# Kernel optimization log

Measured on AMD Instinct MI355X. Metric: run time of the kernel, lower is better.

The kernel has to match this reference:

```python
import jax, jax.numpy as jnp
import numpy as np

N, E, H, G, NF, L = 50000, 600000, 128, 50, 128, 6
NC, NM = 500, 100  # conformers, molecules
CUTOFF = 10.0
OFFSET = jnp.linspace(0.0, CUTOFF, G)                 # GaussianSmearing offsets
COEFF = -0.5 / (CUTOFF / (G - 1)) ** 2
LOG2 = float(np.log(2.0))

def ssp(x):  # ShiftedSoftplus
    return jax.nn.softplus(x) - LOG2

def setup_inputs() -> dict:
    key = jax.random.key(0)
    ks = jax.random.split(key, 24)
    s = 0.05
    return {
        'z': jax.random.randint(ks[0], (N,), 0, 120),
        'pos': jax.random.normal(ks[1], (N, 3), jnp.float32) * 5.0,
        'edge_row': jax.random.randint(ks[2], (E,), 0, N),   # source j
        'edge_col': jax.random.randint(ks[3], (E,), 0, N),   # target i
        'atom_to_conf': jnp.sort(jax.random.randint(ks[4], (N,), 0, NC)),
        'conf_to_mol': jnp.sort(jax.random.randint(ks[5], (NC,), 0, NM)),
        'emb_table': jax.random.normal(ks[6], (120, H)) * s,
        'mlp_w1': jax.random.normal(ks[7], (L, G, NF)) * s,
        'mlp_b1': jnp.zeros((L, NF)),
        'mlp_w2': jax.random.normal(ks[8], (L, NF, NF)) * s,
        'mlp_b2': jnp.zeros((L, NF)),
        'conv_lin1_w': jax.random.normal(ks[9], (L, H, NF)) * s,
        'conv_lin2_w': jax.random.normal(ks[10], (L, NF, H)) * s,
        'conv_lin2_b': jnp.zeros((L, H)),
        'int_lin_w': jax.random.normal(ks[11], (L, H, H)) * s,
        'int_lin_b': jnp.zeros((L, H)),
        'lin1_w': jax.random.normal(ks[12], (H, H)) * s,
        'lin1_b': jnp.zeros((H,)),
        'lin2_w': jax.random.normal(ks[13], (H, H)) * s,
        'lin2_b': jnp.zeros((H,)),
        'head_w1': jax.random.normal(ks[14], (H, H // 2)) * s,
        'head_b1': jnp.zeros((H // 2,)),
        'head_w2': jax.random.normal(ks[15], (H // 2, 1)) * s,
        'head_b2': jnp.zeros((1,)),
    }

def reference(z, pos, edge_row, edge_col, atom_to_conf, conf_to_mol,
              emb_table, mlp_w1, mlp_b1, mlp_w2, mlp_b2,
              conv_lin1_w, conv_lin2_w, conv_lin2_b, int_lin_w, int_lin_b,
              lin1_w, lin1_b, lin2_w, lin2_b,
              head_w1, head_b1, head_w2, head_b2):
    h = emb_table[z]                                         # [N,H]
    # edge geometry (radius graph distances)
    d = jnp.linalg.norm(pos[edge_row] - pos[edge_col], axis=-1)       # [E]
    edge_attr = jnp.exp(COEFF * (d[:, None] - OFFSET[None, :]) ** 2)  # [E,G]
    C = 0.5 * (jnp.cos(d * jnp.pi / CUTOFF) + 1.0)                    # [E]
    for i in range(L):
        # filter network + cosine cutoff
        W = ssp(edge_attr @ mlp_w1[i] + mlp_b1[i]) @ mlp_w2[i] + mlp_b2[i]
        W = W * C[:, None]                                   # [E,NF]
        xf = h @ conv_lin1_w[i]                              # [N,NF]
        msg = xf[edge_row] * W                               # gather x_j, multiply
        agg = jax.ops.segment_sum(msg, edge_col, num_segments=N)  # scatter-add
        x = agg @ conv_lin2_w[i] + conv_lin2_b[i]
        x = ssp(x) @ int_lin_w[i] + int_lin_b[i]
        h = h + x                                            # residual
    h = ssp(h @ lin1_w + lin1_b) @ lin2_w + lin2_b           # [N,H]
    conf_emb = jax.ops.segment_sum(h, atom_to_conf, num_segments=NC)  # [NC,H]
    mol_emb = jax.ops.segment_sum(conf_emb, conf_to_mol, num_segments=NM)  # [NM,H]
    out = (ssp(mol_emb @ head_w1 + head_b1) @ head_w2 + head_b2)[:, 0]  # [NM]
    return out
```

## Files before the change

kernel.cpp:

```cpp
#include <hip/hip_runtime.h>
#include <hip/hip_bf16.h>
#include <hip/hip_fp16.h>
#include <math.h>

#define H_DIM   128
#define NF_DIM  128
#define G_DIM   50
#define L_LAYERS 6
#define TBL     2048
#define DMAX    12.8f
#define CUTOFF_C 10.0f
#define COEFF_C (-0.5f * 49.0f * 49.0f / 100.0f)
#define SCAN_B  256
#define T_PER   16
#define T_PER2  (T_PER + 1)
#define STG_STR 140

typedef __bf16 bf16x8 __attribute__((ext_vector_type(8)));
typedef float  f32x4  __attribute__((ext_vector_type(4)));

__device__ __forceinline__ float sspf(float x) {
    float e = __expf(-fabsf(x));
    return fmaxf(x, 0.0f) + __logf(1.0f + e) - 0.69314718055994530942f;
}

__device__ __forceinline__ unsigned short f2bf(float f) {
    unsigned int u = __float_as_uint(f);
    u = (u + 0x7fffu + ((u >> 16) & 1u)) >> 16;
    return (unsigned short)u;
}

__device__ __forceinline__ float bf2f(unsigned short u) {
    return __uint_as_float(((unsigned int)u) << 16);
}

__device__ __forceinline__ int swz(int c) {
    return c ^ ((c >> 3) & 7) ^ ((c >> 8) & 3);
}

__global__ __launch_bounds__(128) void build_tables(
        const float* __restrict__ w1, const float* __restrict__ b1,
        const float* __restrict__ w2, const float* __restrict__ b2,
        unsigned int* __restrict__ tab2) {
    int l  = blockIdx.x / (TBL / T_PER);
    int t0 = (blockIdx.x % (TBL / T_PER)) * T_PER;
    int f  = threadIdx.x;
    __shared__ float sW1[G_DIM * 128];
    __shared__ float gs[T_PER2][G_DIM + 2];
    __shared__ float sy[T_PER2][130];
    for (int i = f; i < G_DIM * 128; i += 128)
        sW1[i] = w1[(size_t)l * G_DIM * 128 + i];
    if (f < G_DIM) {
        float o = f * (CUTOFF_C / (G_DIM - 1));
#pragma unroll
        for (int u = 0; u < T_PER2; ++u) {
            int t = t0 + u;
            if (t > TBL - 1) t = TBL - 1;
            float dt = t * (DMAX / (TBL - 1));
            float dd = dt - o;
            gs[u][f] = __expf(COEFF_C * dd * dd);
        }
    }
    __syncthreads();
    float y[T_PER2];
    float bb = b1[l * 128 + f];
#pragma unroll
    for (int u = 0; u < T_PER2; ++u) y[u] = bb;
    for (int g = 0; g < G_DIM; ++g) {
        float wv = sW1[g * 128 + f];
#pragma unroll
        for (int u = 0; u < T_PER2; ++u) y[u] += gs[u][g] * wv;
    }
#pragma unroll
    for (int u = 0; u < T_PER2; ++u) sy[u][f] = sspf(y[u]);
    __syncthreads();
    float acc[T_PER2];
    float b2v = b2[l * 128 + f];
#pragma unroll
    for (int u = 0; u < T_PER2; ++u) acc[u] = b2v;
    const float* W2 = w2 + (size_t)l * 16384;
    for (int k = 0; k < 128; ++k) {
        float wv = W2[k * 128 + f];
#pragma unroll
        for (int u = 0; u < T_PER2; ++u) acc[u] += sy[u][k] * wv;
    }
#pragma unroll
    for (int u = 0; u < T_PER; ++u) {
        unsigned int lo = f2bf(acc[u]);
        unsigned int hi = f2bf(acc[u + 1]);
        tab2[((size_t)l * TBL + t0 + u) * 128 + f] = (hi << 16) | lo;
    }
}

__global__ __launch_bounds__(256) void embed_kernel(
        const int* __restrict__ z, const float* __restrict__ emb,
        float* __restrict__ h, int N) {
    int idx = blockIdx.x * blockDim.x + threadIdx.x;
    if (idx >= N * H_DIM) return;
    int n = idx >> 7, f = idx & 127;
    h[idx] = emb[z[n] * H_DIM + f];
}

__global__ __launch_bounds__(256) void prep_wt_sw(
        const float* __restrict__ W, unsigned short* __restrict__ Bsw) {
    int m = blockIdx.x;
    const float* src = W + (size_t)m * 16384;
    unsigned short* dst = Bsw + (size_t)m * 16384;
    for (int i = threadIdx.x; i < 16384; i += 256) {
        int jj = i & 7, lane = (i >> 3) & 63, j = (i >> 9) & 7, ks = i >> 12;
        int n = j * 16 + (lane & 15);
        int k = ks * 32 + ((lane >> 4) & 3) * 8 + jj;
        dst[i] = f2bf(src[k * 128 + n]);
    }
}

__global__ __launch_bounds__(256) void count_kernel(
        const int* __restrict__ ec, int* __restrict__ cnt,
        int* __restrict__ rank, int E) {
    int e = blockIdx.x * blockDim.x + threadIdx.x;
    if (e < E) rank[e] = atomicAdd(&cnt[ec[e]], 1);
}

__global__ __launch_bounds__(SCAN_B) void scan1(
        const int* __restrict__ cnt, int* __restrict__ excl,
        int* __restrict__ bsums, int N) {
    __shared__ int s[SCAN_B];
    int i = blockIdx.x * SCAN_B + threadIdx.x;
    int v = (i < N) ? cnt[i] : 0;
    s[threadIdx.x] = v;
    __syncthreads();
    for (int off = 1; off < SCAN_B; off <<= 1) {
        int t = (threadIdx.x >= off) ? s[threadIdx.x - off] : 0;
        __syncthreads();
        s[threadIdx.x] += t;
        __syncthreads();
    }
    if (i < N) excl[i] = s[threadIdx.x] - v;
    if (threadIdx.x == SCAN_B - 1) bsums[blockIdx.x] = s[SCAN_B - 1];
}

__global__ __launch_bounds__(SCAN_B) void scan2(int* __restrict__ bsums, int nb) {
    __shared__ int s[SCAN_B];
    int v = (threadIdx.x < nb) ? bsums[threadIdx.x] : 0;
    s[threadIdx.x] = v;
    __syncthreads();
    for (int off = 1; off < SCAN_B; off <<= 1) {
        int t = (threadIdx.x >= off) ? s[threadIdx.x - off] : 0;
        __syncthreads();
        s[threadIdx.x] += t;
        __syncthreads();
    }
    if (threadIdx.x < nb) bsums[threadIdx.x] = s[threadIdx.x] - v;
}

__global__ __launch_bounds__(SCAN_B) void scan3(
        const int* __restrict__ excl, const int* __restrict__ bsums,
        int* __restrict__ row_start, int N, int E) {
    int i = blockIdx.x * SCAN_B + threadIdx.x;
    if (i < N) row_start[i] = excl[i] + bsums[blockIdx.x];
    if (i == 0) row_start[N] = E;
}

__global__ __launch_bounds__(256) void build_edges(
        const int* __restrict__ er, const int* __restrict__ ec,
        const float* __restrict__ pos, const int* __restrict__ row_start,
        const int* __restrict__ rank, uint2* __restrict__ ebuf, int E) {
    int e = blockIdx.x * blockDim.x + threadIdx.x;
    if (e >= E) return;
    int r = er[e], c = ec[e];
    float dx = pos[r * 3 + 0] - pos[c * 3 + 0];
    float dy = pos[r * 3 + 1] - pos[c * 3 + 1];
    float dz = pos[r * 3 + 2] - pos[c * 3 + 2];
    float d = sqrtf(dx * dx + dy * dy + dz * dz);
    float C = 0.5f * (cosf(d * (3.14159265358979323846f / CUTOFF_C)) + 1.0f);
    float t = fminf(d, DMAX) * ((TBL - 1) / DMAX);
    int i0 = (int)t;
    if (i0 > TBL - 2) i0 = TBL - 2;
    float fr = t - (float)i0;
    __half2 abh = __floats2half2_rn(C * (1.0f - fr), C * fr);
    ebuf[row_start[c] + rank[e]] =
        make_uint2((unsigned)r | ((unsigned)i0 << 17), *(unsigned*)&abh);
}

__device__ __forceinline__ void edge_acc(
        unsigned ex, unsigned ey, const unsigned int* __restrict__ tab2,
        const unsigned short* __restrict__ xfb, int f4, float4& acc) {
    int r = ex & 0x1ffff, i0 = ex >> 17;
    float2 ab = __half22float2(*(__half2*)&ey);
    uint4 tp = *(const uint4*)(tab2 + (size_t)i0 * 128 + f4);
    const ushort4 xu = *(const ushort4*)(xfb + (size_t)r * 128 + f4);
    acc.x += bf2f(xu.x) * (ab.x * __uint_as_float(tp.x << 16) +
                           ab.y * __uint_as_float(tp.x & 0xffff0000u));
    acc.y += bf2f(xu.y) * (ab.x * __uint_as_float(tp.y << 16) +
                           ab.y * __uint_as_float(tp.y & 0xffff0000u));
    acc.z += bf2f(xu.z) * (ab.x * __uint_as_float(tp.z << 16) +
                           ab.y * __uint_as_float(tp.z & 0xffff0000u));
    acc.w += bf2f(xu.w) * (ab.x * __uint_as_float(tp.w << 16) +
                           ab.y * __uint_as_float(tp.w & 0xffff0000u));
}

__global__ __launch_bounds__(256) void edge_agg(
        const uint2* __restrict__ ebuf, const int* __restrict__ row_start,
        const unsigned short* __restrict__ xfb, const unsigned int* __restrict__ tab2,
        unsigned short* __restrict__ aggb, int N) {
    int tid = threadIdx.x;
    int atom = blockIdx.x * 8 + (tid >> 5);
    if (atom >= N) return;
    int f4 = (tid & 31) * 4;
    float4 a0 = make_float4(0.f, 0.f, 0.f, 0.f);
    float4 a1 = make_float4(0.f, 0.f, 0.f, 0.f);
    float4 a2 = make_float4(0.f, 0.f, 0.f, 0.f);
    float4 a3 = make_float4(0.f, 0.f, 0.f, 0.f);
    int j0 = row_start[atom], j1 = row_start[atom + 1];
    int j = j0;
    if (j < j1 && (j & 1)) {
        uint2 ed = ebuf[j];
        edge_acc(ed.x, ed.y, tab2, xfb, f4, a0);
        ++j;
    }
    for (; j + 3 < j1; j += 4) {
        uint4 e2 = *(const uint4*)(ebuf + j);
        uint4 e3 = *(const uint4*)(ebuf + j + 2);
        edge_acc(e2.x, e2.y, tab2, xfb, f4, a0);
        edge_acc(e2.z, e2.w, tab2, xfb, f4, a1);
        edge_acc(e3.x, e3.y, tab2, xfb, f4, a2);
        edge_acc(e3.z, e3.w, tab2, xfb, f4, a3);
    }
    if (j + 1 < j1) {
        uint4 e2 = *(const uint4*)(ebuf + j);
        edge_acc(e2.x, e2.y, tab2, xfb, f4, a0);
        edge_acc(e2.z, e2.w, tab2, xfb, f4, a1);
        j += 2;
    }
    if (j < j1) {
        uint2 ed = ebuf[j];
        edge_acc(ed.x, ed.y, tab2, xfb, f4, a0);
    }
    a0.x += a1.x + a2.x + a3.x;
    a0.y += a1.y + a2.y + a3.y;
    a0.z += a1.z + a2.z + a3.z;
    a0.w += a1.w + a2.w + a3.w;
    unsigned short o[4] = {f2bf(a0.x), f2bf(a0.y), f2bf(a0.z), f2bf(a0.w)};
    *(uint2*)(aggb + (size_t)atom * 128 + f4) = *(const uint2*)o;
}

#define MODE_BIAS     1
#define MODE_SSP_OUT  2
#define MODE_OUT_BF16 4

__global__ __launch_bounds__(256, 4) void gemm_v2(
        const float* __restrict__ A, const unsigned short* __restrict__ Bsw,
        const float* __restrict__ bias, float* __restrict__ OutF,
        unsigned short* __restrict__ OutB, int M, int mode) {
    __shared__ __align__(16) float smem[64 * 132];
    unsigned short* asw = (unsigned short*)smem;
    int tid = threadIdx.x;
    int m0 = blockIdx.x * 64;

    for (int i = tid; i < 1024; i += 256) {
        int ks = i >> 8, w = (i >> 6) & 3, ln = i & 63;
        int row = m0 + w * 16 + (ln & 15);
        int kb = ks * 32 + (ln >> 4) * 8;
        unsigned short tmp[8];
        if (row < M) {
            const float* ap = A + (size_t)row * 128 + kb;
            float4 v0 = *(const float4*)ap;
            float4 v1 = *(const float4*)(ap + 4);
            tmp[0] = f2bf(v0.x); tmp[1] = f2bf(v0.y);
            tmp[2] = f2bf(v0.z); tmp[3] = f2bf(v0.w);
            tmp[4] = f2bf(v1.x); tmp[5] = f2bf(v1.y);
            tmp[6] = f2bf(v1.z); tmp[7] = f2bf(v1.w);
        } else {
#pragma unroll
            for (int j = 0; j < 8; ++j) tmp[j] = 0;
        }
        *(uint4*)(asw + (size_t)i * 8) = *(const uint4*)tmp;
    }
    __syncthreads();

    int w = tid >> 6, ln = tid & 63;
    int quad = ln >> 4, l15 = ln & 15;
    f32x4 acc[8] = {};
#pragma unroll
    for (int ks = 0; ks < 4; ++ks) {
        bf16x8 af = *(const bf16x8*)(asw + ((ks * 4 + w) * 64 + ln) * 8);
#pragma unroll
        for (int j = 0; j < 8; ++j) {
            bf16x8 bf = *(const bf16x8*)(Bsw + (((ks * 8 + j) * 64) + ln) * 8);
            acc[j] = __builtin_amdgcn_mfma_f32_16x16x32_bf16(af, bf, acc[j], 0, 0, 0);
        }
    }
    __syncthreads();

#pragma unroll
    for (int j = 0; j < 8; ++j) {
        int col = j * 16 + l15;
        float bv = (mode & MODE_BIAS) ? bias[col] : 0.f;
#pragma unroll
        for (int r = 0; r < 4; ++r)
            smem[(w * 16 + quad * 4 + r) * 132 + col] = acc[j][r] + bv;
    }
    __syncthreads();

    for (int i = tid; i < 2048; i += 256) {
        int row = i >> 5, c4 = (i & 31) * 4;
        int grow = m0 + row;
        if (grow >= M) continue;
        float4 v = *(const float4*)(smem + row * 132 + c4);
        if (mode & MODE_SSP_OUT) {
            v.x = sspf(v.x); v.y = sspf(v.y); v.z = sspf(v.z); v.w = sspf(v.w);
        }
        if (mode & MODE_OUT_BF16) {
            unsigned short o[4] = {f2bf(v.x), f2bf(v.y), f2bf(v.z), f2bf(v.w)};
            *(uint2*)(OutB + (size_t)grow * 128 + c4) = *(const uint2*)o;
        } else {
            *(float4*)(OutF + (size_t)grow * 128 + c4) = v;
        }
    }
}

__global__ __launch_bounds__(256, 4) void fused_layer(
        const unsigned short* __restrict__ aggb,
        const unsigned short* __restrict__ B1sw, const float* __restrict__ b1v,
        const unsigned short* __restrict__ B2sw, const float* __restrict__ b2v,
        const unsigned short* __restrict__ B3sw, const float* __restrict__ b3v,
        float* __restrict__ h, unsigned short* __restrict__ xfb_next,
        float* __restrict__ s_out, int M, int last) {
    __shared__ __align__(16) unsigned short frag[8192];
    __shared__ __align__(16) unsigned short stg[64 * STG_STR];
    int tid = threadIdx.x;
    int m0 = blockIdx.x * 64;

    for (int i = tid; i < 1024; i += 256) {
        int ks = i >> 8, w_ = (i >> 6) & 3, ln_ = i & 63;
        int row = m0 + w_ * 16 + (ln_ & 15);
        int kb = ks * 32 + (ln_ >> 4) * 8;
        uint4 v = make_uint4(0, 0, 0, 0);
        if (row < M) v = *(const uint4*)(aggb + (size_t)row * 128 + kb);
        *(uint4*)(frag + swz(i) * 8) = v;
    }
    __syncthreads();

    int w = tid >> 6, ln = tid & 63;
    int quad = ln >> 4, l15 = ln & 15;

    f32x4 acc[8] = {};
#pragma unroll
    for (int ks = 0; ks < 4; ++ks) {
        bf16x8 af = *(const bf16x8*)(frag + swz((ks * 4 + w) * 64 + ln) * 8);
#pragma unroll
        for (int j = 0; j < 8; ++j) {
            bf16x8 bf = *(const bf16x8*)(B1sw + (((ks * 8 + j) * 64) + ln) * 8);
            acc[j] = __builtin_amdgcn_mfma_f32_16x16x32_bf16(af, bf, acc[j], 0, 0, 0);
        }
    }

#pragma unroll
    for (int j = 0; j < 8; ++j) {
        int col = j * 16 + l15;
        float bv = b1v[col];
        int ks2 = j >> 1;
        int quad2 = (col >> 3) & 3;
        int jj = l15 & 7;
        int cbase = (ks2 * 4 + w) * 64 + quad2 * 16 + quad * 4;
#pragma unroll
        for (int r = 0; r < 4; ++r) {
            float s = sspf(acc[j][r] + bv);
            frag[swz(cbase + r) * 8 + jj] = f2bf(s);
        }
    }

    f32x4 acc2[8] = {};
#pragma unroll
    for (int ks = 0; ks < 4; ++ks) {
        bf16x8 af = *(const bf16x8*)(frag + swz((ks * 4 + w) * 64 + ln) * 8);
#pragma unroll
        for (int j = 0; j < 8; ++j) {
            bf16x8 bf = *(const bf16x8*)(B2sw + (((ks * 8 + j) * 64) + ln) * 8);
            acc2[j] = __builtin_amdgcn_mfma_f32_16x16x32_bf16(af, bf, acc2[j], 0, 0, 0);
        }
    }

#pragma unroll
    for (int j = 0; j < 8; ++j) {
        int col = j * 16 + l15;
        float bv = b2v[col];
#pragma unroll
        for (int r = 0; r < 4; ++r)
            stg[(w * 16 + quad * 4 + r) * STG_STR + col] = f2bf(acc2[j][r] + bv);
    }
    __syncthreads();

    for (int i = tid; i < 2048; i += 256) {
        int row = i >> 5, c4 = (i & 31) * 4;
        int grow = m0 + row;
        ushort4 xv = *(const ushort4*)(stg + row * STG_STR + c4);
        float4 v;
        v.x = bf2f(xv.x); v.y = bf2f(xv.y); v.z = bf2f(xv.z); v.w = bf2f(xv.w);
        if (grow < M) {
            float* hp = h + (size_t)grow * 128 + c4;
            float4 o = *(const float4*)hp;
            v.x += o.x; v.y += o.y; v.z += o.z; v.w += o.w;
            *(float4*)hp = v;
        } else {
            v = make_float4(0.f, 0.f, 0.f, 0.f);
        }
        unsigned short t4[4] = {f2bf(v.x), f2bf(v.y), f2bf(v.z), f2bf(v.w)};
        int w_ = row >> 4, l15_ = row & 15;
        int ks = c4 >> 5, q_ = (c4 >> 3) & 3, jj = c4 & 7;
        int c = (ks * 4 + w_) * 64 + q_ * 16 + l15_;
        *(uint2*)(frag + swz(c) * 8 + jj) = *(const uint2*)t4;
    }
    __syncthreads();

    f32x4 acc3[8] = {};
#pragma unroll
    for (int ks = 0; ks < 4; ++ks) {
        bf16x8 af = *(const bf16x8*)(frag + swz((ks * 4 + w) * 64 + ln) * 8);
#pragma unroll
        for (int j = 0; j < 8; ++j) {
            bf16x8 bf = *(const bf16x8*)(B3sw + (((ks * 8 + j) * 64) + ln) * 8);
            acc3[j] = __builtin_amdgcn_mfma_f32_16x16x32_bf16(af, bf, acc3[j], 0, 0, 0);
        }
    }

#pragma unroll
    for (int j = 0; j < 8; ++j) {
        int col = j * 16 + l15;
        float bv = last ? b3v[col] : 0.f;
#pragma unroll
        for (int r = 0; r < 4; ++r) {
            float v = acc3[j][r] + bv;
            if (last) v = sspf(v);
            stg[(w * 16 + quad * 4 + r) * STG_STR + col] = f2bf(v);
        }
    }
    __syncthreads();

    for (int i = tid; i < 2048; i += 256) {
        int row = i >> 5, c4 = (i & 31) * 4;
        int grow = m0 + row;
        if (grow >= M) continue;
        ushort4 s4 = *(const ushort4*)(stg + row * STG_STR + c4);
        if (last) {
            float4 v;
            v.x = bf2f(s4.x); v.y = bf2f(s4.y); v.z = bf2f(s4.z); v.w = bf2f(s4.w);
            *(float4*)(s_out + (size_t)grow * 128 + c4) = v;
        } else {
            *(uint2*)(xfb_next + (size_t)grow * 128 + c4) = *(const uint2*)&s4;
        }
    }
}

#define MR_ATOMS 32
__global__ __launch_bounds__(128) void mol_reduce(
        const float* __restrict__ s, const int* __restrict__ a2c,
        const int* __restrict__ c2m, float* __restrict__ mols,
        int* __restrict__ cnt, int N) {
    int f = threadIdx.x;
    int a0 = blockIdx.x * MR_ATOMS;
    int a1 = min(a0 + MR_ATOMS, N);
    float sum = 0.f;
    int cur = -1, run = 0;
    for (int a = a0; a < a1; ++a) {
        int m = c2m[a2c[a]];
        if (m != cur) {
            if (cur >= 0) {
                unsafeAtomicAdd(&mols[(size_t)cur * H_DIM + f], sum);
                if (f == 0) atomicAdd(&cnt[cur], run);
            }
            cur = m; sum = 0.f; run = 0;
        }
        sum += s[(size_t)a * H_DIM + f];
        ++run;
    }
    if (cur >= 0) {
        unsafeAtomicAdd(&mols[(size_t)cur * H_DIM + f], sum);
        if (f == 0) atomicAdd(&cnt[cur], run);
    }
}

__global__ __launch_bounds__(128) void head_kernel(
        const float* __restrict__ mols, const int* __restrict__ cnt,
        const float* __restrict__ l2w, const float* __restrict__ l2b,
        const float* __restrict__ hw1, const float* __restrict__ hb1,
        const float* __restrict__ hw2, const float* __restrict__ hb2,
        float* __restrict__ out) {
    int m = blockIdx.x, f = threadIdx.x;
    __shared__ float me[H_DIM];
    __shared__ float u[H_DIM / 2];
    const float* ms = mols + (size_t)m * H_DIM;
    float acc = l2b[f] * (float)cnt[m];
#pragma unroll 16
    for (int k = 0; k < H_DIM; ++k) acc += ms[k] * l2w[k * H_DIM + f];
    me[f] = acc;
    __syncthreads();
    if (f < 64) {
        float a2 = hb1[f];
#pragma unroll 16
        for (int k = 0; k < H_DIM; ++k) a2 += me[k] * hw1[k * 64 + f];
        u[f] = sspf(a2);
    }
    __syncthreads();
    if (f == 0) {
        float o = hb2[0];
#pragma unroll 16
        for (int j = 0; j < 64; ++j) o += u[j] * hw2[j];
        out[m] = o;
    }
}

extern "C" void kernel_launch(void* const* d_in, const int* in_sizes, int n_in,
                              void* d_out, int out_size, void* d_ws, size_t ws_size,
                              hipStream_t stream) {
    const int*   z   = (const int*)d_in[0];
    const float* pos = (const float*)d_in[1];
    const int*   er  = (const int*)d_in[2];
    const int*   ec  = (const int*)d_in[3];
    const int*   a2c = (const int*)d_in[4];
    const int*   c2m = (const int*)d_in[5];
    const float* emb = (const float*)d_in[6];
    const float* w1  = (const float*)d_in[7];
    const float* b1  = (const float*)d_in[8];
    const float* w2  = (const float*)d_in[9];
    const float* b2  = (const float*)d_in[10];
    const float* c1w = (const float*)d_in[11];
    const float* c2w = (const float*)d_in[12];
    const float* c2b = (const float*)d_in[13];
    const float* iw  = (const float*)d_in[14];
    const float* ib  = (const float*)d_in[15];
    const float* l1w = (const float*)d_in[16];
    const float* l1b = (const float*)d_in[17];
    const float* l2w = (const float*)d_in[18];
    const float* l2b = (const float*)d_in[19];
    const float* hw1 = (const float*)d_in[20];
    const float* hb1 = (const float*)d_in[21];
    const float* hw2 = (const float*)d_in[22];
    const float* hb2 = (const float*)d_in[23];

    const int N  = in_sizes[0];
    const int E  = in_sizes[2];
    const int NM = out_size;
    float* out = (float*)d_out;

    char* wsp = (char*)d_ws;
    uint2* ebuf = (uint2*)wsp;            wsp += (size_t)E * 8;
    unsigned int* tab2 = (unsigned int*)wsp;  wsp += (size_t)L_LAYERS * TBL * NF_DIM * 4;
    unsigned short* wbt = (unsigned short*)wsp;  wsp += (size_t)19 * 16384 * 2;
    float* h    = (float*)wsp;            wsp += (size_t)N * H_DIM * 4;
    unsigned short* xfb = (unsigned short*)wsp;  wsp += (size_t)N * H_DIM * 2;
    unsigned short* aggb = (unsigned short*)wsp; wsp += (size_t)N * H_DIM * 2;
    float* sbuf = (float*)wsp;            wsp += (size_t)N * H_DIM * 4;
    float* mols = (float*)wsp;            wsp += (size_t)NM * H_DIM * 4;
    int*   cnt_m = (int*)wsp;             wsp += (size_t)NM * 4;
    int*   ccnt  = (int*)wsp;             wsp += (size_t)N * 4;
    int*   row_start = (int*)wsp;         wsp += (size_t)(N + 1) * 4;
    int*   rank  = (int*)wsp;             wsp += (size_t)E * 4;
    int*   bsums = (int*)wsp;             wsp += 256 * 4;
    int*   excl  = (int*)wsp;

    hipMemsetAsync(ccnt, 0, (size_t)N * sizeof(int), stream);
    count_kernel<<<(E + 255) / 256, 256, 0, stream>>>(ec, ccnt, rank, E);
    int nb = (N + SCAN_B - 1) / SCAN_B;
    scan1<<<nb, SCAN_B, 0, stream>>>(ccnt, excl, bsums, N);
    scan2<<<1, SCAN_B, 0, stream>>>(bsums, nb);
    scan3<<<nb, SCAN_B, 0, stream>>>(excl, bsums, row_start, N, E);
    build_edges<<<(E + 255) / 256, 256, 0, stream>>>(
        er, ec, pos, row_start, rank, ebuf, E);

    build_tables<<<L_LAYERS * (TBL / T_PER), 128, 0, stream>>>(w1, b1, w2, b2, tab2);
    embed_kernel<<<(N * H_DIM + 255) / 256, 256, 0, stream>>>(z, emb, h, N);

    prep_wt_sw<<<L_LAYERS, 256, 0, stream>>>(c1w, wbt);
    prep_wt_sw<<<L_LAYERS, 256, 0, stream>>>(c2w, wbt + (size_t)6 * 16384);
    prep_wt_sw<<<L_LAYERS, 256, 0, stream>>>(iw,  wbt + (size_t)12 * 16384);
    prep_wt_sw<<<1,        256, 0, stream>>>(l1w, wbt + (size_t)18 * 16384);

    int gblocks = (N + 63) / 64;
    gemm_v2<<<gblocks, 256, 0, stream>>>(
        h, wbt, nullptr, nullptr, xfb, N, MODE_OUT_BF16);

    for (int l = 0; l < L_LAYERS; ++l) {
        edge_agg<<<(N + 7) / 8, 256, 0, stream>>>(
            ebuf, row_start, xfb, tab2 + (size_t)l * TBL * NF_DIM, aggb, N);
        int last = (l == L_LAYERS - 1);
        const unsigned short* B3 = last ? wbt + (size_t)18 * 16384
                                        : wbt + (size_t)(l + 1) * 16384;
        fused_layer<<<gblocks, 256, 0, stream>>>(
            aggb,
            wbt + (size_t)(6 + l) * 16384,  c2b + (size_t)l * H_DIM,
            wbt + (size_t)(12 + l) * 16384, ib + (size_t)l * H_DIM,
            B3, l1b, h, xfb, sbuf, N, last);
    }

    hipMemsetAsync(mols, 0, (size_t)NM * H_DIM * sizeof(float) + NM * sizeof(int), stream);
    mol_reduce<<<(N + MR_ATOMS - 1) / MR_ATOMS, 128, 0, stream>>>(
        sbuf, a2c, c2m, mols, cnt_m, N);
    head_kernel<<<NM, 128, 0, stream>>>(mols, cnt_m, l2w, l2b, hw1, hb1, hw2, hb2, out);
}
```

Baseline: 681.0 us.

## Store residual hidden state in bf16, merge weight prep, unroll edge loop by eight

The residual stream h now lives in bf16 instead of fp32, which halves its read and write traffic in fused_layer and lets the first GEMM load bf16 directly into swizzled LDS fragments. The four weight-prep launches are merged into one kernel, and the edge aggregation loop is unrolled to eight edges per iteration to put more gathers in flight. The cost is precision: the residual is accumulated in bf16 across six layers, so rounding error builds up.

```diff
diff --git a/kernel.cpp b/kernel.cpp
--- a/kernel.cpp
+++ b/kernel.cpp
@@ -94,17 +94,22 @@
 
 __global__ __launch_bounds__(256) void embed_kernel(
         const int* __restrict__ z, const float* __restrict__ emb,
-        float* __restrict__ h, int N) {
+        unsigned short* __restrict__ hb, int N) {
     int idx = blockIdx.x * blockDim.x + threadIdx.x;
     if (idx >= N * H_DIM) return;
     int n = idx >> 7, f = idx & 127;
-    h[idx] = emb[z[n] * H_DIM + f];
-}
-
-__global__ __launch_bounds__(256) void prep_wt_sw(
-        const float* __restrict__ W, unsigned short* __restrict__ Bsw) {
+    hb[idx] = f2bf(emb[z[n] * H_DIM + f]);
+}
+
+__global__ __launch_bounds__(256) void prep_wt_all(
+        const float* __restrict__ c1w, const float* __restrict__ c2w,
+        const float* __restrict__ iw, const float* __restrict__ l1w,
+        unsigned short* __restrict__ Bsw) {
     int m = blockIdx.x;
-    const float* src = W + (size_t)m * 16384;
+    const float* src = (m < 6)  ? c1w + (size_t)m * 16384
+                     : (m < 12) ? c2w + (size_t)(m - 6) * 16384
+                     : (m < 18) ? iw  + (size_t)(m - 12) * 16384
+                                : l1w;
     unsigned short* dst = Bsw + (size_t)m * 16384;
     for (int i = threadIdx.x; i < 16384; i += 256) {
         int jj = i & 7, lane = (i >> 3) & 63, j = (i >> 9) & 7, ks = i >> 12;
@@ -218,18 +223,33 @@
         edge_acc(ed.x, ed.y, tab2, xfb, f4, a0);
         ++j;
     }
-    for (; j + 3 < j1; j += 4) {
-        uint4 e2 = *(const uint4*)(ebuf + j);
-        uint4 e3 = *(const uint4*)(ebuf + j + 2);
+    for (; j + 7 < j1; j += 8) {
+        uint4 e0 = *(const uint4*)(ebuf + j);
+        uint4 e1 = *(const uint4*)(ebuf + j + 2);
+        uint4 e2 = *(const uint4*)(ebuf + j + 4);
+        uint4 e3 = *(const uint4*)(ebuf + j + 6);
+        edge_acc(e0.x, e0.y, tab2, xfb, f4, a0);
+        edge_acc(e0.z, e0.w, tab2, xfb, f4, a1);
+        edge_acc(e1.x, e1.y, tab2, xfb, f4, a2);
+        edge_acc(e1.z, e1.w, tab2, xfb, f4, a3);
         edge_acc(e2.x, e2.y, tab2, xfb, f4, a0);
         edge_acc(e2.z, e2.w, tab2, xfb, f4, a1);
         edge_acc(e3.x, e3.y, tab2, xfb, f4, a2);
         edge_acc(e3.z, e3.w, tab2, xfb, f4, a3);
     }
+    if (j + 3 < j1) {
+        uint4 e0 = *(const uint4*)(ebuf + j);
+        uint4 e1 = *(const uint4*)(ebuf + j + 2);
+        edge_acc(e0.x, e0.y, tab2, xfb, f4, a0);
+        edge_acc(e0.z, e0.w, tab2, xfb, f4, a1);
+        edge_acc(e1.x, e1.y, tab2, xfb, f4, a2);
+        edge_acc(e1.z, e1.w, tab2, xfb, f4, a3);
+        j += 4;
+    }
     if (j + 1 < j1) {
-        uint4 e2 = *(const uint4*)(ebuf + j);
-        edge_acc(e2.x, e2.y, tab2, xfb, f4, a0);
-        edge_acc(e2.z, e2.w, tab2, xfb, f4, a1);
+        uint4 e0 = *(const uint4*)(ebuf + j);
+        edge_acc(e0.x, e0.y, tab2, xfb, f4, a0);
+        edge_acc(e0.z, e0.w, tab2, xfb, f4, a1);
         j += 2;
     }
     if (j < j1) {
@@ -244,78 +264,48 @@
     *(uint2*)(aggb + (size_t)atom * 128 + f4) = *(const uint2*)o;
 }
 
-#define MODE_BIAS     1
-#define MODE_SSP_OUT  2
-#define MODE_OUT_BF16 4
-
-__global__ __launch_bounds__(256, 4) void gemm_v2(
-        const float* __restrict__ A, const unsigned short* __restrict__ Bsw,
-        const float* __restrict__ bias, float* __restrict__ OutF,
-        unsigned short* __restrict__ OutB, int M, int mode) {
-    __shared__ __align__(16) float smem[64 * 132];
-    unsigned short* asw = (unsigned short*)smem;
+__global__ __launch_bounds__(256, 4) void gemm_l0(
+        const unsigned short* __restrict__ hb, const unsigned short* __restrict__ Bsw,
+        unsigned short* __restrict__ xfb, int M) {
+    __shared__ __align__(16) unsigned short frag[8192];
+    __shared__ __align__(16) unsigned short stg[64 * STG_STR];
     int tid = threadIdx.x;
     int m0 = blockIdx.x * 64;
-
     for (int i = tid; i < 1024; i += 256) {
-        int ks = i >> 8, w = (i >> 6) & 3, ln = i & 63;
-        int row = m0 + w * 16 + (ln & 15);
-        int kb = ks * 32 + (ln >> 4) * 8;
-        unsigned short tmp[8];
-        if (row < M) {
-            const float* ap = A + (size_t)row * 128 + kb;
-            float4 v0 = *(const float4*)ap;
-            float4 v1 = *(const float4*)(ap + 4);
-            tmp[0] = f2bf(v0.x); tmp[1] = f2bf(v0.y);
-            tmp[2] = f2bf(v0.z); tmp[3] = f2bf(v0.w);
-            tmp[4] = f2bf(v1.x); tmp[5] = f2bf(v1.y);
-            tmp[6] = f2bf(v1.z); tmp[7] = f2bf(v1.w);
-        } else {
-#pragma unroll
-            for (int j = 0; j < 8; ++j) tmp[j] = 0;
-        }
-        *(uint4*)(asw + (size_t)i * 8) = *(const uint4*)tmp;
-    }
-    __syncthreads();
-
+        int ks = i >> 8, w_ = (i >> 6) & 3, ln_ = i & 63;
+        int row = m0 + w_ * 16 + (ln_ & 15);
+        int kb = ks * 32 + (ln_ >> 4) * 8;
+        uint4 v = make_uint4(0, 0, 0, 0);
+        if (row < M) v = *(const uint4*)(hb + (size_t)row * 128 + kb);
+        *(uint4*)(frag + swz(i) * 8) = v;
+    }
+    __syncthreads();
     int w = tid >> 6, ln = tid & 63;
     int quad = ln >> 4, l15 = ln & 15;
     f32x4 acc[8] = {};
 #pragma unroll
     for (int ks = 0; ks < 4; ++ks) {
-        bf16x8 af = *(const bf16x8*)(asw + ((ks * 4 + w) * 64 + ln) * 8);
+        bf16x8 af = *(const bf16x8*)(frag + swz((ks * 4 + w) * 64 + ln) * 8);
 #pragma unroll
         for (int j = 0; j < 8; ++j) {
             bf16x8 bf = *(const bf16x8*)(Bsw + (((ks * 8 + j) * 64) + ln) * 8);
             acc[j] = __builtin_amdgcn_mfma_f32_16x16x32_bf16(af, bf, acc[j], 0, 0, 0);
         }
     }
-    __syncthreads();
-
 #pragma unroll
     for (int j = 0; j < 8; ++j) {
         int col = j * 16 + l15;
-        float bv = (mode & MODE_BIAS) ? bias[col] : 0.f;
 #pragma unroll
         for (int r = 0; r < 4; ++r)
-            smem[(w * 16 + quad * 4 + r) * 132 + col] = acc[j][r] + bv;
-    }
-    __syncthreads();
-
+            stg[(w * 16 + quad * 4 + r) * STG_STR + col] = f2bf(acc[j][r]);
+    }
+    __syncthreads();
     for (int i = tid; i < 2048; i += 256) {
         int row = i >> 5, c4 = (i & 31) * 4;
         int grow = m0 + row;
         if (grow >= M) continue;
-        float4 v = *(const float4*)(smem + row * 132 + c4);
-        if (mode & MODE_SSP_OUT) {
-            v.x = sspf(v.x); v.y = sspf(v.y); v.z = sspf(v.z); v.w = sspf(v.w);
-        }
-        if (mode & MODE_OUT_BF16) {
-            unsigned short o[4] = {f2bf(v.x), f2bf(v.y), f2bf(v.z), f2bf(v.w)};
-            *(uint2*)(OutB + (size_t)grow * 128 + c4) = *(const uint2*)o;
-        } else {
-            *(float4*)(OutF + (size_t)grow * 128 + c4) = v;
-        }
+        ushort4 s4 = *(const ushort4*)(stg + row * STG_STR + c4);
+        *(uint2*)(xfb + (size_t)grow * 128 + c4) = *(const uint2*)&s4;
     }
 }
 
@@ -324,7 +314,7 @@
         const unsigned short* __restrict__ B1sw, const float* __restrict__ b1v,
         const unsigned short* __restrict__ B2sw, const float* __restrict__ b2v,
         const unsigned short* __restrict__ B3sw, const float* __restrict__ b3v,
-        float* __restrict__ h, unsigned short* __restrict__ xfb_next,
+        unsigned short* __restrict__ hb, unsigned short* __restrict__ xfb_next,
         float* __restrict__ s_out, int M, int last) {
     __shared__ __align__(16) unsigned short frag[8192];
     __shared__ __align__(16) unsigned short stg[64 * STG_STR];
@@ -395,17 +385,18 @@
         int row = i >> 5, c4 = (i & 31) * 4;
         int grow = m0 + row;
         ushort4 xv = *(const ushort4*)(stg + row * STG_STR + c4);
-        float4 v;
-        v.x = bf2f(xv.x); v.y = bf2f(xv.y); v.z = bf2f(xv.z); v.w = bf2f(xv.w);
+        unsigned short t4[4];
         if (grow < M) {
-            float* hp = h + (size_t)grow * 128 + c4;
-            float4 o = *(const float4*)hp;
-            v.x += o.x; v.y += o.y; v.z += o.z; v.w += o.w;
-            *(float4*)hp = v;
+            unsigned short* hp = hb + (size_t)grow * 128 + c4;
+            ushort4 hv = *(const ushort4*)hp;
+            t4[0] = f2bf(bf2f(hv.x) + bf2f(xv.x));
+            t4[1] = f2bf(bf2f(hv.y) + bf2f(xv.y));
+            t4[2] = f2bf(bf2f(hv.z) + bf2f(xv.z));
+            t4[3] = f2bf(bf2f(hv.w) + bf2f(xv.w));
+            *(uint2*)hp = *(const uint2*)t4;
         } else {
-            v = make_float4(0.f, 0.f, 0.f, 0.f);
-        }
-        unsigned short t4[4] = {f2bf(v.x), f2bf(v.y), f2bf(v.z), f2bf(v.w)};
+            t4[0] = t4[1] = t4[2] = t4[3] = 0;
+        }
         int w_ = row >> 4, l15_ = row & 15;
         int ks = c4 >> 5, q_ = (c4 >> 3) & 3, jj = c4 & 7;
         int c = (ks * 4 + w_) * 64 + q_ * 16 + l15_;
@@ -547,7 +538,7 @@
     uint2* ebuf = (uint2*)wsp;            wsp += (size_t)E * 8;
     unsigned int* tab2 = (unsigned int*)wsp;  wsp += (size_t)L_LAYERS * TBL * NF_DIM * 4;
     unsigned short* wbt = (unsigned short*)wsp;  wsp += (size_t)19 * 16384 * 2;
-    float* h    = (float*)wsp;            wsp += (size_t)N * H_DIM * 4;
+    unsigned short* hb  = (unsigned short*)wsp;  wsp += (size_t)N * H_DIM * 2;
     unsigned short* xfb = (unsigned short*)wsp;  wsp += (size_t)N * H_DIM * 2;
     unsigned short* aggb = (unsigned short*)wsp; wsp += (size_t)N * H_DIM * 2;
     float* sbuf = (float*)wsp;            wsp += (size_t)N * H_DIM * 4;
@@ -569,16 +560,11 @@
         er, ec, pos, row_start, rank, ebuf, E);
 
     build_tables<<<L_LAYERS * (TBL / T_PER), 128, 0, stream>>>(w1, b1, w2, b2, tab2);
-    embed_kernel<<<(N * H_DIM + 255) / 256, 256, 0, stream>>>(z, emb, h, N);
-
-    prep_wt_sw<<<L_LAYERS, 256, 0, stream>>>(c1w, wbt);
-    prep_wt_sw<<<L_LAYERS, 256, 0, stream>>>(c2w, wbt + (size_t)6 * 16384);
-    prep_wt_sw<<<L_LAYERS, 256, 0, stream>>>(iw,  wbt + (size_t)12 * 16384);
-    prep_wt_sw<<<1,        256, 0, stream>>>(l1w, wbt + (size_t)18 * 16384);
+    embed_kernel<<<(N * H_DIM + 255) / 256, 256, 0, stream>>>(z, emb, hb, N);
+    prep_wt_all<<<19, 256, 0, stream>>>(c1w, c2w, iw, l1w, wbt);
 
     int gblocks = (N + 63) / 64;
-    gemm_v2<<<gblocks, 256, 0, stream>>>(
-        h, wbt, nullptr, nullptr, xfb, N, MODE_OUT_BF16);
+    gemm_l0<<<gblocks, 256, 0, stream>>>(hb, wbt, xfb, N);
 
     for (int l = 0; l < L_LAYERS; ++l) {
         edge_agg<<<(N + 7) / 8, 256, 0, stream>>>(
@@ -590,7 +576,7 @@
             aggb,
             wbt + (size_t)(6 + l) * 16384,  c2b + (size_t)l * H_DIM,
             wbt + (size_t)(12 + l) * 16384, ib + (size_t)l * H_DIM,
-            B3, l1b, h, xfb, sbuf, N, last);
+            B3, l1b, hb, xfb, sbuf, N, last);
     }
 
     hipMemsetAsync(mols, 0, (size_t)NM * H_DIM * sizeof(float) + NM * sizeof(int), stream);
```

Measured after the change: 677.7 us. No clear change (-0.5%).
